# Kernel tuning notes

Measured on AMD Instinct MI355X. Metric: run time of the kernel, lower is better.

Reference implementation:

```python
import jax, jax.numpy as jnp
import numpy as np
from jax import lax

NUM_CLASSES = 80
TOPK = 1000
CONF_THRESH = 0.05
NMS_THRESH = 0.6
MAX_COORD = 4096.0  # > any box coordinate; used for class-aware NMS offset trick
N_ANCHORS = 262144


def setup_inputs() -> dict:
    key = jax.random.key(0)
    k1, k2, k3 = jax.random.split(key, 3)
    # classification logits; shift down so sigmoid scores are mostly below conf_thresh
    cls_pred = jax.random.normal(k1, (1, N_ANCHORS, NUM_CLASSES), jnp.float32) * 2.0 - 2.0
    # valid xyxy boxes in absolute pixel coords (image ~1024)
    xy = jax.random.uniform(k2, (1, N_ANCHORS, 2), jnp.float32) * 1000.0
    wh = jax.random.uniform(k3, (1, N_ANCHORS, 2), jnp.float32) * 200.0 + 4.0
    box_pred = jnp.concatenate([xy, xy + wh], axis=-1)
    return {"cls_pred": cls_pred, "box_pred": box_pred, "img_h": 1024, "img_w": 1024}


def _pairwise_iou(b):
    # b: [K, 4] xyxy -> [K, K] IoU
    x1, y1, x2, y2 = b[:, 0], b[:, 1], b[:, 2], b[:, 3]
    area = (x2 - x1) * (y2 - y1)
    ix1 = jnp.maximum(x1[:, None], x1[None, :])
    iy1 = jnp.maximum(y1[:, None], y1[None, :])
    ix2 = jnp.minimum(x2[:, None], x2[None, :])
    iy2 = jnp.minimum(y2[:, None], y2[None, :])
    inter = jnp.clip(ix2 - ix1, 0.0) * jnp.clip(iy2 - iy1, 0.0)
    return inter / (area[:, None] + area[None, :] - inter + 1e-9)


def reference(cls_pred, box_pred, img_h, img_w):
    cls_p = cls_pred[0]          # [N, C]
    box_p = box_pred[0]          # [N, 4]
    # sigmoid + flatten + descending sort + slice(topk)  ==  top_k on flat scores
    scores_all = jax.nn.sigmoid(cls_p).reshape(-1)            # [N*C]
    top_scores, top_idxs = lax.top_k(scores_all, TOPK)        # sorted descending
    valid = top_scores > CONF_THRESH                          # keep mask (fixed size)
    labels = top_idxs % NUM_CLASSES
    anchor_idxs = top_idxs // NUM_CLASSES
    boxes = box_p[anchor_idxs]                                # [K, 4]

    # class-aware (per-class) greedy NMS via coordinate offset trick
    offset = labels.astype(boxes.dtype)[:, None] * MAX_COORD
    iou = _pairwise_iou(boxes + offset)                       # [K, K]
    idx = jnp.arange(TOPK)

    def body(i, keep):
        sup = keep[i] & (iou[i] > NMS_THRESH) & (idx > i)
        return keep & ~sup

    keep = lax.fori_loop(0, TOPK, body, valid)

    # normalize boxes to [0, 1] by image size and clip (as inference_single_image)
    scale = jnp.array([img_w, img_h, img_w, img_h], dtype=boxes.dtype)
    boxes_norm = jnp.clip(boxes / scale, 0.0, 1.0)

    scores_out = jnp.where(keep, top_scores, 0.0)
    return boxes_norm, scores_out, labels, keep
```

## Files before the change

### kernel.cpp

```cpp
#include <hip/hip_runtime.h>
#include <stdint.h>

#define NUM_CLASSES 80u
#define TOPK 1000
#define CONF_T 0.05f
#define NMS_T 0.6f
#define MAX_COORD 4096.0f
#define TARGET 1152u
#define CAP 49152u
#define SRVCAP 2048u
#define STATIC_F 4.0f
#define STATIC_KEY 0xC0800000u
#define NBINS 4096
#define BINSH 13
#define LCAP 512u
#define PBLK 1024u

typedef unsigned long long ull;
typedef ull ull2 __attribute__((ext_vector_type(2)));

__device__ __forceinline__ uint32_t fkey(float x) {
  uint32_t k = __float_as_uint(x);
  return (k & 0x80000000u) ? ~k : (k | 0x80000000u);
}

__device__ __forceinline__ uint32_t suffix_scan_256(uint32_t v, uint32_t* part,
                                                    int t) {
  int lane = t & 63, wid = t >> 6;
#pragma unroll
  for (int off = 1; off < 64; off <<= 1) {
    uint32_t x = __shfl_down(v, off);
    if (lane + off < 64) v += x;
  }
  if (lane == 0) part[wid] = v;
  __syncthreads();
  if (wid == 0 && lane < 4) {
    uint32_t pv = part[lane];
#pragma unroll
    for (int off = 1; off < 4; off <<= 1) {
      uint32_t x = __shfl_down(pv, off);
      if (lane + off < 4) pv += x;
    }
    part[lane] = pv;
  }
  __syncthreads();
  uint32_t after = (wid < 3) ? part[wid + 1] : 0u;
  return v + after;
}

template <int NBINSX>
__device__ __forceinline__ void pick_bin(const uint32_t* hl, uint32_t target,
                                         int t, uint32_t* part, uint32_t* binS,
                                         uint32_t* AS, uint32_t* cntS) {
  const int CH = NBINSX / 256;
  uint32_t s = 0;
#pragma unroll
  for (int j = 0; j < CH; ++j) s += hl[t * CH + j];
  uint32_t incl = suffix_scan_256(s, part, t);
  uint32_t after = incl - s;
  if (incl >= target && after < target) {
    uint32_t cum = after;
    for (int j = CH - 1; j >= 0; --j) {
      uint32_t h = hl[t * CH + j];
      if (cum + h >= target) { *binS = (uint32_t)(t * CH + j); *AS = cum; *cntS = h; break; }
      cum += h;
    }
  }
}

__global__ void __launch_bounds__(256) kz(uint32_t* hist, uint32_t* sel,
                                          float* out, float* topScore) {
  int g = blockIdx.x * 256 + threadIdx.x;
  hist[g] = 0u;
  if (g < 16) sel[g] = 0u;
  for (int i = g; i < 4000; i += 4096) out[i] = 0.0f;
  if (g < 1000) { out[5000 + g] = 0.0f; topScore[g] = 0.0f; }
}

__global__ void __launch_bounds__(256) kA(const float4* __restrict__ cls, int n4,
                                          uint32_t* __restrict__ sel,
                                          uint32_t* __restrict__ hist,
                                          uint32_t* __restrict__ candKey,
                                          uint32_t* __restrict__ candIdx) {
  __shared__ uint32_t lk[LCAP];
  __shared__ uint32_t li[LCAP];
  __shared__ uint32_t lcnt, gbase;
  if (threadIdx.x == 0) lcnt = 0u;
  __syncthreads();
  int stride = gridDim.x * blockDim.x;
  for (int i = blockIdx.x * blockDim.x + threadIdx.x; i < n4; i += stride) {
    float4 v = cls[i];
    float f4[4] = {v.x, v.y, v.z, v.w};
#pragma unroll
    for (int c = 0; c < 4; ++c) {
      if (f4[c] >= STATIC_F) {
        uint32_t k = fkey(f4[c]);
        uint32_t b = (k - STATIC_KEY) >> BINSH; if (b > NBINS - 1u) b = NBINS - 1u;
        atomicAdd(&hist[b], 1u);
        uint32_t p = atomicAdd(&lcnt, 1u);
        if (p < LCAP) { lk[p] = k; li[p] = (uint32_t)i * 4u + c; }
        else {
          uint32_t gp = atomicAdd(&sel[2], 1u);
          if (gp < CAP) { candKey[gp] = k; candIdx[gp] = (uint32_t)i * 4u + c; }
        }
      }
    }
  }
  __syncthreads();
  uint32_t c = lcnt; if (c > LCAP) c = LCAP;
  if (threadIdx.x == 0 && c) gbase = atomicAdd(&sel[2], c);
  __syncthreads();
  for (uint32_t i = threadIdx.x; i < c; i += 256u) {
    uint32_t gp = gbase + i;
    if (gp < CAP) { candKey[gp] = lk[i]; candIdx[gp] = li[i]; }
  }
}

__global__ void __launch_bounds__(256) kSel(
    const float4* __restrict__ cls4, int n4,
    uint32_t* __restrict__ sel, const uint32_t* __restrict__ hist,
    const uint32_t* __restrict__ candKey, const uint32_t* __restrict__ candIdx,
    ull* __restrict__ srv) {
  __shared__ uint32_t hl[NBINS];
  __shared__ uint32_t part[16];
  __shared__ uint32_t sk_[PBLK];
  __shared__ uint32_t si_[PBLK];
  __shared__ uint32_t lcnt, gbase, binS, AS, cntS;
  int t = threadIdx.x;
  uint32_t n = sel[2];
  bool fb = (n < TARGET) || (n > CAP);

  if (!fb) {
    for (int i = t; i < NBINS; i += 256) hl[i] = hist[i];
    if (t == 0) { lcnt = 0u; binS = 0u; AS = 0u; cntS = 0u; }
    __syncthreads();
    pick_bin<NBINS>(hl, TARGET, t, part, &binS, &AS, &cntS);
    __syncthreads();
    uint32_t T;
    if (AS + cntS > SRVCAP)
      T = STATIC_KEY + ((binS + 1u) << BINSH);
    else
      T = STATIC_KEY + (binS << BINSH);
    uint32_t stride = gridDim.x * blockDim.x;
    for (uint32_t i = blockIdx.x * 256u + (uint32_t)t; i < n; i += stride) {
      uint32_t k = candKey[i];
      if (k >= T) {
        uint32_t p = atomicAdd(&lcnt, 1u);
        if (p < PBLK) { sk_[p] = k; si_[p] = candIdx[i]; }
      }
    }
    __syncthreads();
    uint32_t c = lcnt; if (c > PBLK) c = PBLK;
    if (t == 0 && c) gbase = atomicAdd(&sel[4], c);
    __syncthreads();
    for (uint32_t i = t; i < c; i += 256u) {
      uint32_t k = sk_[i];
      float x = __uint_as_float(k & 0x7fffffffu);
      float p = 1.0f / (1.0f + expf(-x));
      uint32_t pos = gbase + i;
      if (pos < SRVCAP)
        srv[pos] = ((ull)__float_as_uint(p) << 32) | (ull)(uint32_t)(~si_[i]);
    }
  } else {
    if (blockIdx.x != 0) return;
    for (int i = t; i < NBINS; i += 256) hl[i] = 0u;
    if (t == 0) { binS = 0u; AS = 0u; cntS = 0u; }
    __syncthreads();
    for (int i = t; i < n4; i += 256) {
      float4 v = cls4[i];
      atomicAdd(&hl[fkey(v.x) >> 20], 1u);
      atomicAdd(&hl[fkey(v.y) >> 20], 1u);
      atomicAdd(&hl[fkey(v.z) >> 20], 1u);
      atomicAdd(&hl[fkey(v.w) >> 20], 1u);
    }
    __syncthreads();
    pick_bin<NBINS>(hl, TARGET, t, part, &binS, &AS, &cntS);
    __syncthreads();
    uint32_t b20 = binS, A = AS;
    for (int i = t; i < 1024; i += 256) hl[i] = 0u;
    if (t == 0) { binS = 0u; }
    __syncthreads();
    for (int i = t; i < n4; i += 256) {
      float4 v = cls4[i];
      uint32_t k4[4] = {fkey(v.x), fkey(v.y), fkey(v.z), fkey(v.w)};
#pragma unroll
      for (int c2 = 0; c2 < 4; ++c2)
        if ((k4[c2] >> 20) == b20) atomicAdd(&hl[(k4[c2] >> 10) & 1023u], 1u);
    }
    __syncthreads();
    uint32_t rem = TARGET - A;
    pick_bin<1024>(hl, rem, t, part, &binS, &AS, &cntS);
    __syncthreads();
    uint32_t T = (b20 << 20) | (binS << 10);
    for (int i = t; i < n4; i += 256) {
      float4 v = cls4[i];
      uint32_t k4[4] = {fkey(v.x), fkey(v.y), fkey(v.z), fkey(v.w)};
#pragma unroll
      for (int c2 = 0; c2 < 4; ++c2) {
        uint32_t k = k4[c2];
        if (k >= T) {
          uint32_t pos = atomicAdd(&sel[4], 1u);
          if (pos < SRVCAP) {
            float x = (k & 0x80000000u) ? __uint_as_float(k & 0x7fffffffu)
                                        : __uint_as_float(~k);
            float p = 1.0f / (1.0f + expf(-x));
            uint32_t idx = (uint32_t)i * 4u + c2;
            srv[pos] = ((ull)__float_as_uint(p) << 32) | (ull)(uint32_t)(~idx);
          }
        }
      }
    }
  }
}

__global__ void __launch_bounds__(64) kF2(
    const float* __restrict__ box, const int* __restrict__ ph,
    const int* __restrict__ pw, const uint32_t* __restrict__ sel,
    const ull* __restrict__ srv, float* __restrict__ out,
    float* __restrict__ topScore, float* __restrict__ obox) {
  __shared__ __align__(16) ull sk[SRVCAP];
  int t = threadIdx.x;
  uint32_t scount = sel[4]; if (scount > SRVCAP) scount = SRVCAP;
  uint32_t pad = (scount + 1u) & ~1u;
  for (uint32_t i = t; i < pad; i += 64u) sk[i] = (i < scount) ? srv[i] : 0ull;
  __syncthreads();
  uint32_t i = blockIdx.x * 64u + (uint32_t)t;
  if (i >= scount) return;
  ull my = sk[i];
  uint32_t rank = 0;
#pragma unroll 4
  for (uint32_t j = 0; j < pad; j += 2u) {
    ull2 v = *reinterpret_cast<const ull2*>(&sk[j]);
    rank += (v.x > my) + (v.y > my);
  }
  if (rank >= TOPK) return;
  uint32_t idx = ~(uint32_t)my;
  float p = __uint_as_float((uint32_t)(my >> 32));
  uint32_t label = idx % NUM_CLASSES;
  uint32_t anchor = idx / NUM_CLASSES;
  float W = (float)pw[0], H = (float)ph[0];
  float b0 = box[anchor * 4u + 0u], b1 = box[anchor * 4u + 1u];
  float b2 = box[anchor * 4u + 2u], b3 = box[anchor * 4u + 3u];
  out[rank * 4 + 0] = fminf(fmaxf(b0 / W, 0.0f), 1.0f);
  out[rank * 4 + 1] = fminf(fmaxf(b1 / H, 0.0f), 1.0f);
  out[rank * 4 + 2] = fminf(fmaxf(b2 / W, 0.0f), 1.0f);
  out[rank * 4 + 3] = fminf(fmaxf(b3 / H, 0.0f), 1.0f);
  out[5000 + rank] = (float)label;
  topScore[rank] = p;
  float off = (float)label * MAX_COORD;
  obox[rank * 4 + 0] = b0 + off; obox[rank * 4 + 1] = b1 + off;
  obox[rank * 4 + 2] = b2 + off; obox[rank * 4 + 3] = b3 + off;
}

__global__ void kG(const float* __restrict__ obox, ull* __restrict__ masks) {
  int i = blockIdx.x;
  float x1i = obox[i * 4 + 0], y1i = obox[i * 4 + 1];
  float x2i = obox[i * 4 + 2], y2i = obox[i * 4 + 3];
  float ai = (x2i - x1i) * (y2i - y1i);
  for (int base = 0; base < 1024; base += 256) {
    int jj = base + (int)threadIdx.x;
    bool bit = false;
    if (jj < TOPK && jj > i) {
      float x1j = obox[jj * 4 + 0], y1j = obox[jj * 4 + 1];
      float x2j = obox[jj * 4 + 2], y2j = obox[jj * 4 + 3];
      float aj = (x2j - x1j) * (y2j - y1j);
      float ix1 = fmaxf(x1i, x1j), iy1 = fmaxf(y1i, y1j);
      float ix2 = fminf(x2i, x2j), iy2 = fminf(y2i, y2j);
      float iw = fmaxf(ix2 - ix1, 0.0f), ih = fmaxf(iy2 - iy1, 0.0f);
      float inter = iw * ih;
      float iou = inter / (ai + aj - inter + 1e-9f);
      bit = iou > NMS_T;
    }
    ull m = __ballot(bit);
    if ((threadIdx.x & 63u) == 0u) masks[i * 16 + (jj >> 6)] = m;
  }
}

__global__ void __launch_bounds__(256) kH(const float* __restrict__ topScore,
                                          const ull* __restrict__ masks,
                                          float* __restrict__ out) {
  __shared__ ull lmask[TOPK * 16];
  __shared__ uint32_t nzrow[TOPK];
  __shared__ ull keepsh[16];
  int t = threadIdx.x;
  for (int i = t; i < TOPK; i += 256) nzrow[i] = 0u;
  if (t < 16) keepsh[t] = 0ull;
  __syncthreads();
  for (int i = t; i < TOPK * 16; i += 256) {
    ull m = masks[i];
    lmask[i] = m;
    if (m) atomicOr(&nzrow[i >> 4], 1u);
  }
  for (int base = 0; base < 1024; base += 256) {
    int r = base + t;
    bool v = (r < TOPK) && (topScore[r] > CONF_T);
    ull b = __ballot(v);
    if ((t & 63) == 0) keepsh[(base >> 6) + (t >> 6)] = b;
  }
  __syncthreads();
  if (t < 64) {
    ull kw = (t < 16) ? keepsh[t] : 0ull;
    ull nzw = 0ull;
    if (t < 16) {
      for (int b = 0; b < 64; ++b) {
        int r = t * 64 + b;
        if (r < TOPK && nzrow[r]) nzw |= 1ull << b;
      }
    }
    for (int w = 0; w < 16; ++w) {
      ull cur = __shfl(kw, w) & __shfl(nzw, w);
      while (cur) {
        int b = __ffsll((long long)cur) - 1;
        int i = w * 64 + b;
        if (t < 16) kw &= ~lmask[i * 16 + t];
        ull nk = __shfl(kw, w);
        cur = nk & __shfl(nzw, w);
        cur &= (b == 63) ? 0ull : (~0ull << (b + 1));
      }
    }
    if (t < 16) keepsh[t] = kw;
  }
  __syncthreads();
  for (int r = t; r < TOPK; r += 256) {
    bool k = (keepsh[r >> 6] >> (r & 63)) & 1ull;
    float s = topScore[r];
    out[4000 + r] = k ? s : 0.0f;
    out[6000 + r] = k ? 1.0f : 0.0f;
  }
}

extern "C" void kernel_launch(void* const* d_in, const int* in_sizes, int n_in,
                              void* d_out, int out_size, void* d_ws, size_t ws_size,
                              hipStream_t stream) {
  const float* cls = (const float*)d_in[0];
  const float* box = (const float*)d_in[1];
  const int* ph = (const int*)d_in[2];
  const int* pw = (const int*)d_in[3];
  float* out = (float*)d_out;
  int n = in_sizes[0];

  uint8_t* w = (uint8_t*)d_ws;
  uint32_t* hist    = (uint32_t*)(w);
  uint32_t* sel     = (uint32_t*)(w + 16384);
  uint32_t* candKey = (uint32_t*)(w + 20480);
  uint32_t* candIdx = (uint32_t*)(w + 20480 + (size_t)CAP * 4);
  ull*      srv     = (ull*)     (w + 20480 + (size_t)CAP * 8);
  float*    topScore= (float*)   (w + 20480 + (size_t)CAP * 8 + 16384);
  float*    obox    = (float*)   (w + 20480 + (size_t)CAP * 8 + 16384 + 4096);
  ull*      masks   = (ull*)     (w + 20480 + (size_t)CAP * 8 + 16384 + 4096 + 16384);

  kz  <<<16, 256, 0, stream>>>(hist, sel, out, topScore);
  kA  <<<1024, 256, 0, stream>>>((const float4*)cls, n / 4, sel, hist, candKey, candIdx);
  kSel<<<64, 256, 0, stream>>>((const float4*)cls, n / 4, sel, hist, candKey, candIdx, srv);
  kF2 <<<SRVCAP / 64, 64, 0, stream>>>(box, ph, pw, sel, srv, out, topScore, obox);
  kG  <<<TOPK, 256, 0, stream>>>(obox, masks);
  kH  <<<1, 256, 0, stream>>>(topScore, masks, out);
}
```

Before: 210.2 us.

## Software-pipeline kA loads, register-scan kSel histogram, add row-summary bitmask for NMS

The candidate-scan kernel kA now double-buffers five float4 loads per thread ahead of processing and launches twice as many blocks with an occupancy hint, to keep more memory requests in flight on the 84 MB logits read. kSel picks the threshold bin from histogram values held in registers instead of first copying the histogram to shared memory. kF2 now uses 256-thread blocks. kG writes a per-row bitmask of non-empty 64-bit mask words, which kH uses to skip loading zero mask words and to build its non-zero-row bitmap. The changes add register pressure and a small extra workspace buffer.

```diff
diff --git a/kernel.cpp b/kernel.cpp
--- a/kernel.cpp
+++ b/kernel.cpp
@@ -77,35 +77,85 @@
   if (g < 1000) { out[5000 + g] = 0.0f; topScore[g] = 0.0f; }
 }
 
-__global__ void __launch_bounds__(256) kA(const float4* __restrict__ cls, int n4,
-                                          uint32_t* __restrict__ sel,
-                                          uint32_t* __restrict__ hist,
-                                          uint32_t* __restrict__ candKey,
-                                          uint32_t* __restrict__ candIdx) {
+__device__ __forceinline__ void kA_proc1(float f, uint32_t eidx,
+                                         uint32_t* __restrict__ sel,
+                                         uint32_t* __restrict__ hist,
+                                         uint32_t* __restrict__ candKey,
+                                         uint32_t* __restrict__ candIdx,
+                                         uint32_t* lk, uint32_t* li,
+                                         uint32_t* lcnt) {
+  if (f >= STATIC_F) {
+    uint32_t k = fkey(f);
+    uint32_t bb = (k - STATIC_KEY) >> BINSH;
+    if (bb > NBINS - 1u) bb = NBINS - 1u;
+    atomicAdd(&hist[bb], 1u);
+    uint32_t p = atomicAdd(lcnt, 1u);
+    if (p < LCAP) { lk[p] = k; li[p] = eidx; }
+    else {
+      uint32_t gp = atomicAdd(&sel[2], 1u);
+      if (gp < CAP) { candKey[gp] = k; candIdx[gp] = eidx; }
+    }
+  }
+}
+
+__global__ void __launch_bounds__(256, 4) kA(const float4* __restrict__ cls,
+                                             int n4,
+                                             uint32_t* __restrict__ sel,
+                                             uint32_t* __restrict__ hist,
+                                             uint32_t* __restrict__ candKey,
+                                             uint32_t* __restrict__ candIdx) {
   __shared__ uint32_t lk[LCAP];
   __shared__ uint32_t li[LCAP];
   __shared__ uint32_t lcnt, gbase;
   if (threadIdx.x == 0) lcnt = 0u;
   __syncthreads();
-  int stride = gridDim.x * blockDim.x;
-  for (int i = blockIdx.x * blockDim.x + threadIdx.x; i < n4; i += stride) {
-    float4 v = cls[i];
-    float f4[4] = {v.x, v.y, v.z, v.w};
-#pragma unroll
-    for (int c = 0; c < 4; ++c) {
-      if (f4[c] >= STATIC_F) {
-        uint32_t k = fkey(f4[c]);
-        uint32_t b = (k - STATIC_KEY) >> BINSH; if (b > NBINS - 1u) b = NBINS - 1u;
-        atomicAdd(&hist[b], 1u);
-        uint32_t p = atomicAdd(&lcnt, 1u);
-        if (p < LCAP) { lk[p] = k; li[p] = (uint32_t)i * 4u + c; }
-        else {
-          uint32_t gp = atomicAdd(&sel[2], 1u);
-          if (gp < CAP) { candKey[gp] = k; candIdx[gp] = (uint32_t)i * 4u + c; }
-        }
-      }
-    }
-  }
+  const uint32_t nth = gridDim.x * blockDim.x;
+  const uint32_t gid = blockIdx.x * blockDim.x + threadIdx.x;
+
+#define LDB_(R, mo)                                                          \
+  _Pragma("unroll") for (int u = 0; u < 5; ++u) R[u] =                       \
+      cls[gid + ((mo) + (uint32_t)u) * nth];
+#define PROC_(R, mo)                                                         \
+  _Pragma("unroll") for (int u = 0; u < 5; ++u) {                            \
+    uint32_t e = (gid + ((mo) + (uint32_t)u) * nth) * 4u;                    \
+    kA_proc1(R[u].x, e + 0u, sel, hist, candKey, candIdx, lk, li, &lcnt);    \
+    kA_proc1(R[u].y, e + 1u, sel, hist, candKey, candIdx, lk, li, &lcnt);    \
+    kA_proc1(R[u].z, e + 2u, sel, hist, candKey, candIdx, lk, li, &lcnt);    \
+    kA_proc1(R[u].w, e + 3u, sel, hist, candKey, candIdx, lk, li, &lcnt);    \
+  }
+
+  if ((uint32_t)n4 % nth == 0u) {
+    const uint32_t T = (uint32_t)n4 / nth;
+    const uint32_t nb = T / 5u;
+    float4 A[5], B[5];
+    if (nb) LDB_(A, 0u);
+    for (uint32_t b = 0; b < nb; b += 2u) {
+      bool hasB = (b + 1u < nb);
+      if (hasB) LDB_(B, (b + 1u) * 5u);
+      PROC_(A, b * 5u);
+      if (b + 2u < nb) LDB_(A, (b + 2u) * 5u);
+      if (hasB) PROC_(B, (b + 1u) * 5u);
+    }
+    for (uint32_t m = nb * 5u; m < T; ++m) {
+      float4 v = cls[gid + m * nth];
+      uint32_t e = (gid + m * nth) * 4u;
+      kA_proc1(v.x, e + 0u, sel, hist, candKey, candIdx, lk, li, &lcnt);
+      kA_proc1(v.y, e + 1u, sel, hist, candKey, candIdx, lk, li, &lcnt);
+      kA_proc1(v.z, e + 2u, sel, hist, candKey, candIdx, lk, li, &lcnt);
+      kA_proc1(v.w, e + 3u, sel, hist, candKey, candIdx, lk, li, &lcnt);
+    }
+  } else {
+    for (uint32_t i = gid; i < (uint32_t)n4; i += nth) {
+      float4 v = cls[i];
+      uint32_t e = i * 4u;
+      kA_proc1(v.x, e + 0u, sel, hist, candKey, candIdx, lk, li, &lcnt);
+      kA_proc1(v.y, e + 1u, sel, hist, candKey, candIdx, lk, li, &lcnt);
+      kA_proc1(v.z, e + 2u, sel, hist, candKey, candIdx, lk, li, &lcnt);
+      kA_proc1(v.w, e + 3u, sel, hist, candKey, candIdx, lk, li, &lcnt);
+    }
+  }
+#undef LDB_
+#undef PROC_
   __syncthreads();
   uint32_t c = lcnt; if (c > LCAP) c = LCAP;
   if (threadIdx.x == 0 && c) gbase = atomicAdd(&sel[2], c);
@@ -131,10 +181,30 @@
   bool fb = (n < TARGET) || (n > CAP);
 
   if (!fb) {
-    for (int i = t; i < NBINS; i += 256) hl[i] = hist[i];
+    uint32_t hh[16];
+    const uint4* h4 = (const uint4*)hist;
+#pragma unroll
+    for (int q = 0; q < 4; ++q) {
+      uint4 v = h4[t * 4 + q];
+      hh[q * 4 + 0] = v.x; hh[q * 4 + 1] = v.y;
+      hh[q * 4 + 2] = v.z; hh[q * 4 + 3] = v.w;
+    }
     if (t == 0) { lcnt = 0u; binS = 0u; AS = 0u; cntS = 0u; }
-    __syncthreads();
-    pick_bin<NBINS>(hl, TARGET, t, part, &binS, &AS, &cntS);
+    uint32_t s = 0;
+#pragma unroll
+    for (int j = 0; j < 16; ++j) s += hh[j];
+    uint32_t incl = suffix_scan_256(s, part, t);
+    uint32_t after = incl - s;
+    if (incl >= TARGET && after < TARGET) {
+      uint32_t cum = after;
+#pragma unroll
+      for (int j = 15; j >= 0; --j) {
+        if (cum + hh[j] >= TARGET) {
+          binS = (uint32_t)(t * 16 + j); AS = cum; cntS = hh[j]; break;
+        }
+        cum += hh[j];
+      }
+    }
     __syncthreads();
     uint32_t T;
     if (AS + cntS > SRVCAP)
@@ -213,7 +283,7 @@
   }
 }
 
-__global__ void __launch_bounds__(64) kF2(
+__global__ void __launch_bounds__(256) kF2(
     const float* __restrict__ box, const int* __restrict__ ph,
     const int* __restrict__ pw, const uint32_t* __restrict__ sel,
     const ull* __restrict__ srv, float* __restrict__ out,
@@ -222,9 +292,9 @@
   int t = threadIdx.x;
   uint32_t scount = sel[4]; if (scount > SRVCAP) scount = SRVCAP;
   uint32_t pad = (scount + 1u) & ~1u;
-  for (uint32_t i = t; i < pad; i += 64u) sk[i] = (i < scount) ? srv[i] : 0ull;
-  __syncthreads();
-  uint32_t i = blockIdx.x * 64u + (uint32_t)t;
+  for (uint32_t i = t; i < pad; i += 256u) sk[i] = (i < scount) ? srv[i] : 0ull;
+  __syncthreads();
+  uint32_t i = blockIdx.x * 256u + (uint32_t)t;
   if (i >= scount) return;
   ull my = sk[i];
   uint32_t rank = 0;
@@ -252,8 +322,12 @@
   obox[rank * 4 + 2] = b2 + off; obox[rank * 4 + 3] = b3 + off;
 }
 
-__global__ void kG(const float* __restrict__ obox, ull* __restrict__ masks) {
+__global__ void kG(const float* __restrict__ obox, ull* __restrict__ masks,
+                   uint32_t* __restrict__ rowsum) {
+  __shared__ uint32_t rsS;
   int i = blockIdx.x;
+  if (threadIdx.x == 0) rsS = 0u;
+  __syncthreads();
   float x1i = obox[i * 4 + 0], y1i = obox[i * 4 + 1];
   float x2i = obox[i * 4 + 2], y2i = obox[i * 4 + 3];
   float ai = (x2i - x1i) * (y2i - y1i);
@@ -272,24 +346,28 @@
       bit = iou > NMS_T;
     }
     ull m = __ballot(bit);
-    if ((threadIdx.x & 63u) == 0u) masks[i * 16 + (jj >> 6)] = m;
-  }
+    if ((threadIdx.x & 63u) == 0u) {
+      masks[i * 16 + (jj >> 6)] = m;
+      if (m) atomicOr(&rsS, 1u << (jj >> 6));
+    }
+  }
+  __syncthreads();
+  if (threadIdx.x == 0) rowsum[i] = rsS;
 }
 
 __global__ void __launch_bounds__(256) kH(const float* __restrict__ topScore,
                                           const ull* __restrict__ masks,
+                                          const uint32_t* __restrict__ rowsum,
                                           float* __restrict__ out) {
   __shared__ ull lmask[TOPK * 16];
-  __shared__ uint32_t nzrow[TOPK];
+  __shared__ uint32_t rsL[TOPK];
   __shared__ ull keepsh[16];
   int t = threadIdx.x;
-  for (int i = t; i < TOPK; i += 256) nzrow[i] = 0u;
+  for (int i = t; i < TOPK; i += 256) rsL[i] = rowsum[i];
   if (t < 16) keepsh[t] = 0ull;
   __syncthreads();
   for (int i = t; i < TOPK * 16; i += 256) {
-    ull m = masks[i];
-    lmask[i] = m;
-    if (m) atomicOr(&nzrow[i >> 4], 1u);
+    lmask[i] = ((rsL[i >> 4] >> (i & 15)) & 1u) ? masks[i] : 0ull;
   }
   for (int base = 0; base < 1024; base += 256) {
     int r = base + t;
@@ -304,7 +382,7 @@
     if (t < 16) {
       for (int b = 0; b < 64; ++b) {
         int r = t * 64 + b;
-        if (r < TOPK && nzrow[r]) nzw |= 1ull << b;
+        if (r < TOPK && rsL[r]) nzw |= 1ull << b;
       }
     }
     for (int w = 0; w < 16; ++w) {
@@ -348,11 +426,12 @@
   float*    topScore= (float*)   (w + 20480 + (size_t)CAP * 8 + 16384);
   float*    obox    = (float*)   (w + 20480 + (size_t)CAP * 8 + 16384 + 4096);
   ull*      masks   = (ull*)     (w + 20480 + (size_t)CAP * 8 + 16384 + 4096 + 16384);
+  uint32_t* rowsum  = (uint32_t*)(w + 20480 + (size_t)CAP * 8 + 16384 + 4096 + 16384 + 131072);
 
   kz  <<<16, 256, 0, stream>>>(hist, sel, out, topScore);
-  kA  <<<1024, 256, 0, stream>>>((const float4*)cls, n / 4, sel, hist, candKey, candIdx);
+  kA  <<<2048, 256, 0, stream>>>((const float4*)cls, n / 4, sel, hist, candKey, candIdx);
   kSel<<<64, 256, 0, stream>>>((const float4*)cls, n / 4, sel, hist, candKey, candIdx, srv);
-  kF2 <<<SRVCAP / 64, 64, 0, stream>>>(box, ph, pw, sel, srv, out, topScore, obox);
-  kG  <<<TOPK, 256, 0, stream>>>(obox, masks);
-  kH  <<<1, 256, 0, stream>>>(topScore, masks, out);
-}
+  kF2 <<<SRVCAP / 256, 256, 0, stream>>>(box, ph, pw, sel, srv, out, topScore, obox);
+  kG  <<<TOPK, 256, 0, stream>>>(obox, masks, rowsum);
+  kH  <<<1, 256, 0, stream>>>(topScore, masks, rowsum, out);
+}
```

After: 194.6 us. 1.08x faster.
